# Performance work log

Measured on AMD Instinct MI355X. Metric: run time of the kernel, lower is better.

## Reference

```python
import jax, jax.numpy as jnp
import numpy as np


def _cdist(p1, p2):
    # Euclidean cdist via the matmul expansion (matches torch.cdist p=2 fast path):
    # ||a-b||^2 = ||a||^2 + ||b||^2 - 2 a.b ; clamp tiny negatives before sqrt.
    sq1 = jnp.sum(p1 * p1, axis=-1, keepdims=True)        # (N, 1)
    sq2 = jnp.sum(p2 * p2, axis=-1, keepdims=True).T      # (1, M)
    d2 = sq1 + sq2 - 2.0 * (p1 @ p2.T)                    # (N, M)
    return jnp.sqrt(jnp.maximum(d2, 0.0))


def setup_inputs() -> dict:
    key = jax.random.key(0)
    k1, k2 = jax.random.split(key)
    N, M = 16384, 16384
    points1 = jax.random.normal(k1, (N, 3), dtype=jnp.float32)
    points2 = jax.random.normal(k2, (M, 3), dtype=jnp.float32)
    return {"points1": points1, "points2": points2}


def reference(points1, points2):
    dist = _cdist(points1, points2)                        # (N, M)
    min1 = jnp.min(dist, axis=1)                           # (N,) nearest in points2
    min2 = jnp.min(dist, axis=0)                           # (M,) nearest in points1
    return jnp.sum(min1) + jnp.sum(min2)
```

## Files before the change

kernel.cpp:

```cpp
#include <hip/hip_runtime.h>
#include <math.h>


typedef _Float16 half8    __attribute__((ext_vector_type(8)));
typedef float    floatx16 __attribute__((ext_vector_type(16)));

constexpr int NPTS = 16384;
constexpr int ROWS = 128;
constexpr int BLK  = 1024;

__device__ __forceinline__ uint2 pack_point(const float* __restrict__ P, int j)
{
    float x = P[3*j], y = P[3*j+1], z = P[3*j+2];
    _Float16 hx = (_Float16)x, hy = (_Float16)y, hz = (_Float16)z;
    float qx = (float)hx, qy = (float)hy, qz = (float)hz;
    _Float16 hw = (_Float16)(qx*qx + qy*qy + qz*qz);
    union { _Float16 h[4]; uint2 u; } p;
    p.h[0] = hx; p.h[1] = hy; p.h[2] = hz; p.h[3] = hw;
    return p.u;
}

__global__ __launch_bounds__(BLK, 4) void chamfer_all_kernel(
    const float* __restrict__ P1, const float* __restrict__ P2,
    float* __restrict__ out, int n1, int n2)
{
    __shared__ uint2 sB[NPTS];
    __shared__ float sRowMin[4][ROWS];
    __shared__ float sRed[ROWS];

    const int dir   = blockIdx.z;
    const float* PA = dir == 0 ? P1 : P2;
    const float* PB = dir == 0 ? P2 : P1;
    const int nA    = dir == 0 ? n1 : n2;
    const int nB    = dir == 0 ? n2 : n1;

    const int tid  = threadIdx.x;
    const int wave = tid >> 6;
    const int lane = tid & 63;
    const int n    = lane & 31;
    const int g    = lane >> 5;
    const bool g0  = (g == 0);
    const int wr   = wave & 3;
    const int wq   = wave >> 2;

    for (int j = tid; j < NPTS; j += BLK) {
        int jj = j < nB ? j : nB - 1;
        sB[j] = pack_point(PB, jj);
    }

    const _Float16 h0 = (_Float16)0.0f;
    half8 af;
    {
        int arow = blockIdx.x * ROWS + wr * 32 + n;
        int j = arow < nA ? arow : nA - 1;
        union { uint2 u; _Float16 h[4]; } au; au.u = pack_point(PA, j);
        const _Float16 m2 = (_Float16)(-2.0f);
        af[0] = g0 ? (_Float16)(au.h[0] * m2) : h0;
        af[1] = g0 ? (_Float16)(au.h[1] * m2) : h0;
        af[2] = g0 ? (_Float16)(au.h[2] * m2) : h0;
        af[3] = g0 ? (_Float16)1.0f : h0;
        af[4] = g0 ? au.h[3] : h0;
        af[5] = h0; af[6] = h0; af[7] = h0;
    }

    __syncthreads();

    floatx16 rowmin;
#pragma unroll
    for (int r = 0; r < 16; ++r) rowmin[r] = 1e30f;
    const floatx16 zacc = {};

    union BF { half8 v; unsigned u[4]; uint2 lo; };
    BF bu0, bu1;
    { union { _Float16 h[2]; unsigned u; } q;
      q.h[0] = (_Float16)1.0f; q.h[1] = h0;
      bu0.u[2] = q.u; bu0.u[3] = 0u;
      bu1.u[2] = q.u; bu1.u[3] = 0u; }

    constexpr int QLEN = NPTS >> 2;
    constexpr int NT   = QLEN / 64;
    const uint2* qbase = sB + wq * QLEN + n;
    uint2 c0 = qbase[0], c1 = qbase[32];

    for (int bt = 0; bt < NT; ++bt) {
        const uint2* pn = qbase + (bt + 1 < NT ? (bt + 1) * 64 : 0);
        uint2 f0 = pn[0], f1 = pn[32];

        bu0.lo = c0;
        bu1.lo = c1;

        floatx16 d0 = __builtin_amdgcn_mfma_f32_32x32x16_f16(af, bu0.v, zacc, 0, 0, 0);
        floatx16 d1 = __builtin_amdgcn_mfma_f32_32x32x16_f16(af, bu1.v, zacc, 0, 0, 0);

#pragma unroll
        for (int r = 0; r < 16; ++r)
            rowmin[r] = fminf(fminf(rowmin[r], d0[r]), d1[r]);

        c0 = f0; c1 = f1;
    }

#pragma unroll
    for (int mask = 1; mask <= 16; mask <<= 1)
#pragma unroll
        for (int r = 0; r < 16; ++r)
            rowmin[r] = fminf(rowmin[r], __shfl_xor(rowmin[r], mask));

    if (n == 0) {
#pragma unroll
        for (int r = 0; r < 16; ++r) {
            int rr = wr * 32 + g * 4 + ((r & 3) + 8 * (r >> 2));
            sRowMin[wq][rr] = rowmin[r];
        }
    }
    __syncthreads();

    if (tid < ROWS) {
        float m = fminf(fminf(sRowMin[0][tid], sRowMin[1][tid]),
                        fminf(sRowMin[2][tid], sRowMin[3][tid]));
        int grow = blockIdx.x * ROWS + tid;
        sRed[tid] = (grow < nA) ? sqrtf(fmaxf(m, 0.0f)) : 0.0f;
    }
    __syncthreads();

    if (tid < 64) {
        float v = sRed[tid] + sRed[tid + 64];
#pragma unroll
        for (int mask = 1; mask <= 32; mask <<= 1)
            v += __shfl_xor(v, mask);
        if (tid == 0) atomicAdd(out, v);
    }
}

extern "C" void kernel_launch(void* const* d_in, const int* in_sizes, int n_in,
                              void* d_out, int out_size, void* d_ws, size_t ws_size,
                              hipStream_t stream) {
    const float* P1 = (const float*)d_in[0];
    const float* P2 = (const float*)d_in[1];
    const int n1 = in_sizes[0] / 3;
    const int n2 = in_sizes[1] / 3;
    float* out = (float*)d_out;

    hipMemsetAsync(out, 0, sizeof(float), stream);

    dim3 grid(NPTS / ROWS, 1, 2);
    chamfer_all_kernel<<<grid, BLK, 0, stream>>>(P1, P2, out, n1, n2);
}
```

Before: 78.13 us.

## Split B-point sweep into halves with partial mins and separate reduce kernel

Each block now loads only half of the opposing point set (8192 points) into shared memory, and the grid doubles along y to cover both halves. Per-row partial minima go to a workspace buffer, and a second kernel combines the two halves, applies sqrt and does the sum with atomics. This halves LDS use per block, doubles block count, and raises the launch-bounds occupancy hint, so more blocks can be resident. The cost is an extra kernel launch, a workspace round-trip, and removal of the software prefetch in the inner loop.

```diff
diff --git a/kernel.cpp b/kernel.cpp
--- a/kernel.cpp
+++ b/kernel.cpp
@@ -6,6 +6,7 @@
 typedef float    floatx16 __attribute__((ext_vector_type(16)));
 
 constexpr int NPTS = 16384;
+constexpr int HALF = 8192;
 constexpr int ROWS = 128;
 constexpr int BLK  = 1024;
 
@@ -20,15 +21,15 @@
     return p.u;
 }
 
-__global__ __launch_bounds__(BLK, 4) void chamfer_all_kernel(
+__global__ __launch_bounds__(BLK, 8) void chamfer_sweep_kernel(
     const float* __restrict__ P1, const float* __restrict__ P2,
-    float* __restrict__ out, int n1, int n2)
+    float* __restrict__ part, int n1, int n2)
 {
-    __shared__ uint2 sB[NPTS];
+    __shared__ uint2 sB[HALF];
     __shared__ float sRowMin[4][ROWS];
-    __shared__ float sRed[ROWS];
 
     const int dir   = blockIdx.z;
+    const int half  = blockIdx.y;
     const float* PA = dir == 0 ? P1 : P2;
     const float* PB = dir == 0 ? P2 : P1;
     const int nA    = dir == 0 ? n1 : n2;
@@ -43,8 +44,9 @@
     const int wr   = wave & 3;
     const int wq   = wave >> 2;
 
-    for (int j = tid; j < NPTS; j += BLK) {
-        int jj = j < nB ? j : nB - 1;
+    for (int j = tid; j < HALF; j += BLK) {
+        int jg = half * HALF + j;
+        int jj = jg < nB ? jg : nB - 1;
         sB[j] = pack_point(PB, jj);
     }
 
@@ -77,26 +79,21 @@
       bu0.u[2] = q.u; bu0.u[3] = 0u;
       bu1.u[2] = q.u; bu1.u[3] = 0u; }
 
-    constexpr int QLEN = NPTS >> 2;
+    constexpr int QLEN = HALF >> 2;
     constexpr int NT   = QLEN / 64;
     const uint2* qbase = sB + wq * QLEN + n;
-    uint2 c0 = qbase[0], c1 = qbase[32];
+    for (int bt = 0; bt < NT; ++bt) {
+        const uint2* p = qbase + bt * 64;
+        bu0.lo = p[0];
+        bu1.lo = p[32];
 
-    for (int bt = 0; bt < NT; ++bt) {
-        const uint2* pn = qbase + (bt + 1 < NT ? (bt + 1) * 64 : 0);
-        uint2 f0 = pn[0], f1 = pn[32];
+        floatx16 d = __builtin_amdgcn_mfma_f32_32x32x16_f16(af, bu0.v, zacc, 0, 0, 0);
+#pragma unroll
+        for (int r = 0; r < 16; ++r) rowmin[r] = fminf(rowmin[r], d[r]);
 
-        bu0.lo = c0;
-        bu1.lo = c1;
-
-        floatx16 d0 = __builtin_amdgcn_mfma_f32_32x32x16_f16(af, bu0.v, zacc, 0, 0, 0);
-        floatx16 d1 = __builtin_amdgcn_mfma_f32_32x32x16_f16(af, bu1.v, zacc, 0, 0, 0);
-
+        d = __builtin_amdgcn_mfma_f32_32x32x16_f16(af, bu1.v, zacc, 0, 0, 0);
 #pragma unroll
-        for (int r = 0; r < 16; ++r)
-            rowmin[r] = fminf(fminf(rowmin[r], d0[r]), d1[r]);
-
-        c0 = f0; c1 = f1;
+        for (int r = 0; r < 16; ++r) rowmin[r] = fminf(rowmin[r], d[r]);
     }
 
 #pragma unroll
@@ -118,17 +115,30 @@
         float m = fminf(fminf(sRowMin[0][tid], sRowMin[1][tid]),
                         fminf(sRowMin[2][tid], sRowMin[3][tid]));
         int grow = blockIdx.x * ROWS + tid;
-        sRed[tid] = (grow < nA) ? sqrtf(fmaxf(m, 0.0f)) : 0.0f;
+        if (grow < nA)
+            part[(size_t)(((dir << 14) + grow) << 1) + half] = m;
     }
+}
+
+__global__ __launch_bounds__(256) void reduce_kernel(
+    const float* __restrict__ part, float* __restrict__ out,
+    int n1, int n2)
+{
+    __shared__ float s[256];
+    int rr = blockIdx.x * 256 + threadIdx.x;
+    int dir = rr >> 14, row = rr & 16383;
+    float acc = 0.0f;
+    if (row < (dir == 0 ? n1 : n2)) {
+        const float2 v = ((const float2*)part)[rr];
+        acc = sqrtf(fmaxf(fminf(v.x, v.y), 0.0f));
+    }
+    s[threadIdx.x] = acc;
     __syncthreads();
-
-    if (tid < 64) {
-        float v = sRed[tid] + sRed[tid + 64];
-#pragma unroll
-        for (int mask = 1; mask <= 32; mask <<= 1)
-            v += __shfl_xor(v, mask);
-        if (tid == 0) atomicAdd(out, v);
+    for (int w = 128; w > 0; w >>= 1) {
+        if (threadIdx.x < w) s[threadIdx.x] += s[threadIdx.x + w];
+        __syncthreads();
     }
+    if (threadIdx.x == 0) atomicAdd(out, s[0]);
 }
 
 extern "C" void kernel_launch(void* const* d_in, const int* in_sizes, int n_in,
@@ -138,10 +148,14 @@
     const float* P2 = (const float*)d_in[1];
     const int n1 = in_sizes[0] / 3;
     const int n2 = in_sizes[1] / 3;
-    float* out = (float*)d_out;
+    float* part = (float*)d_ws;
+    float* out  = (float*)d_out;
 
     hipMemsetAsync(out, 0, sizeof(float), stream);
 
-    dim3 grid(NPTS / ROWS, 1, 2);
-    chamfer_all_kernel<<<grid, BLK, 0, stream>>>(P1, P2, out, n1, n2);
+    {
+        dim3 grid(NPTS / ROWS, 2, 2);
+        chamfer_sweep_kernel<<<grid, BLK, 0, stream>>>(P1, P2, part, n1, n2);
+    }
+    reduce_kernel<<<(2 * NPTS) / 256, 256, 0, stream>>>(part, out, n1, n2);
 }
```

Result: slower. 81.24 us (+4.0%).

## Software-pipeline MFMA and min-fold with inline asm and sched barriers

Applied to the files above, without the earlier changes.

Restructures the inner loop into a two-stage ping-pong so the MFMAs for tile t+1 are issued before the min-fold of tile t's results. Inline asm MFMAs and sched_barrier stop the compiler from serialising the fold behind the MFMA latency. The aim is to hide MFMA latency behind VALU fminf work. The cost is more accumulator registers live at once, which could reduce occupancy. Inline asm also skips the compiler's hazard handling, so correctness depends on the hardware resolving MFMA result dependencies.

```diff
diff --git a/kernel.cpp b/kernel.cpp
--- a/kernel.cpp
+++ b/kernel.cpp
@@ -68,7 +68,9 @@
     floatx16 rowmin;
 #pragma unroll
     for (int r = 0; r < 16; ++r) rowmin[r] = 1e30f;
-    const floatx16 zacc = {};
+    floatx16 zacc;
+#pragma unroll
+    for (int r = 0; r < 16; ++r) zacc[r] = 0.0f;
 
     union BF { half8 v; unsigned u[4]; uint2 lo; };
     BF bu0, bu1;
@@ -79,25 +81,40 @@
 
     constexpr int QLEN = NPTS >> 2;
     constexpr int NT   = QLEN / 64;
-    const uint2* qbase = sB + wq * QLEN + n;
-    uint2 c0 = qbase[0], c1 = qbase[32];
+    const uint2* qb = sB + wq * QLEN + n;
 
-    for (int bt = 0; bt < NT; ++bt) {
-        const uint2* pn = qbase + (bt + 1 < NT ? (bt + 1) * 64 : 0);
-        uint2 f0 = pn[0], f1 = pn[32];
+#define LOADB(t)  do { bu0.lo = qb[(t) * 64]; bu1.lo = qb[(t) * 64 + 32]; } while (0)
+#define MFMA_PAIR(D0, D1) do { \
+    asm("v_mfma_f32_32x32x16_f16 %0, %1, %2, %3" \
+        : "=&v"(D0) : "v"(af), "v"(bu0.v), "v"(zacc)); \
+    asm("v_mfma_f32_32x32x16_f16 %0, %1, %2, %3" \
+        : "=&v"(D1) : "v"(af), "v"(bu1.v), "v"(zacc)); } while (0)
+#define FOLD(P0, P1) do { \
+    _Pragma("unroll") \
+    for (int r = 0; r < 16; ++r) \
+        rowmin[r] = fminf(fminf(rowmin[r], (P0)[r]), (P1)[r]); } while (0)
 
-        bu0.lo = c0;
-        bu1.lo = c1;
-
-        floatx16 d0 = __builtin_amdgcn_mfma_f32_32x32x16_f16(af, bu0.v, zacc, 0, 0, 0);
-        floatx16 d1 = __builtin_amdgcn_mfma_f32_32x32x16_f16(af, bu1.v, zacc, 0, 0, 0);
-
-#pragma unroll
-        for (int r = 0; r < 16; ++r)
-            rowmin[r] = fminf(fminf(rowmin[r], d0[r]), d1[r]);
-
-        c0 = f0; c1 = f1;
+    floatx16 pA0, pA1, pB0, pB1;
+    LOADB(0);
+    MFMA_PAIR(pA0, pA1);
+    for (int t = 1; t < NT - 1; t += 2) {
+        LOADB(t);
+        MFMA_PAIR(pB0, pB1);
+        __builtin_amdgcn_sched_barrier(0);
+        FOLD(pA0, pA1);
+        LOADB(t + 1);
+        MFMA_PAIR(pA0, pA1);
+        __builtin_amdgcn_sched_barrier(0);
+        FOLD(pB0, pB1);
     }
+    LOADB(NT - 1);
+    MFMA_PAIR(pB0, pB1);
+    __builtin_amdgcn_sched_barrier(0);
+    FOLD(pA0, pA1);
+    FOLD(pB0, pB1);
+#undef LOADB
+#undef MFMA_PAIR
+#undef FOLD
 
 #pragma unroll
     for (int mask = 1; mask <= 16; mask <<= 1)
```

New measurement: 77.06 us. Within noise of the previous version (-1.4%).

## Hand-schedule MFMA/min inner loop in inline asm with double-buffered B fragments

Applied to the files above, without the earlier changes.

Replaces the compiler-generated inner loop with inline assembly that pins MFMA outputs and B fragments to fixed VGPRs. LDS reads for the next tile are issued before the min3 fold of the previous MFMA results, and the loop alternates between two B register sets. The constant 1.0/0 halves of the B fragments are written once instead of every iteration. The code hardcodes register numbers and uses s_nop padding for MFMA result hazards, so correctness depends on the exact register clobbers and hazard timing.

```diff
diff --git a/kernel.cpp b/kernel.cpp
--- a/kernel.cpp
+++ b/kernel.cpp
@@ -19,6 +19,91 @@
     p.h[0] = hx; p.h[1] = hy; p.h[2] = hz; p.h[3] = hw;
     return p.u;
 }
+
+#define CLB "v32","v33","v34","v35","v36","v37","v38","v39", \
+            "v40","v41","v42","v43","v44","v45","v46","v47", \
+            "v48","v49","v50","v51","v52","v53","v54","v55", \
+            "v56","v57","v58","v59","v60","v61","v62","v63", \
+            "v64","v65","v66","v67","v68","v69","v70","v71", \
+            "v72","v73","v74","v75","v76","v77","v78","v79"
+
+#define PRO_ASM \
+    "ds_read_b64 v[64:65], %0\n\t" \
+    "ds_read_b64 v[68:69], %0 offset:256\n\t" \
+    "v_mov_b32 v66, 0x3c00\n\t" \
+    "v_mov_b32 v67, 0\n\t" \
+    "v_mov_b32 v70, 0x3c00\n\t" \
+    "v_mov_b32 v71, 0\n\t" \
+    "v_mov_b32 v74, 0x3c00\n\t" \
+    "v_mov_b32 v75, 0\n\t" \
+    "v_mov_b32 v78, 0x3c00\n\t" \
+    "v_mov_b32 v79, 0\n\t" \
+    "v_add_u32 %0, 512, %0\n\t" \
+    "s_waitcnt lgkmcnt(0)\n\t" \
+    "v_mfma_f32_32x32x16_f16 v[32:47], %1, v[64:67], %2\n\t" \
+    "v_mfma_f32_32x32x16_f16 v[48:63], %1, v[68:71], %2"
+
+#define FOLD16 \
+    "v_min3_f32 %1, %1, v32, v48\n\t" \
+    "v_min3_f32 %2, %2, v33, v49\n\t" \
+    "v_min3_f32 %3, %3, v34, v50\n\t" \
+    "v_min3_f32 %4, %4, v35, v51\n\t" \
+    "v_min3_f32 %5, %5, v36, v52\n\t" \
+    "v_min3_f32 %6, %6, v37, v53\n\t" \
+    "v_min3_f32 %7, %7, v38, v54\n\t" \
+    "v_min3_f32 %8, %8, v39, v55\n\t" \
+    "v_min3_f32 %9, %9, v40, v56\n\t" \
+    "v_min3_f32 %10, %10, v41, v57\n\t" \
+    "v_min3_f32 %11, %11, v42, v58\n\t" \
+    "v_min3_f32 %12, %12, v43, v59\n\t" \
+    "v_min3_f32 %13, %13, v44, v60\n\t" \
+    "v_min3_f32 %14, %14, v45, v61\n\t" \
+    "v_min3_f32 %15, %15, v46, v62\n\t" \
+    "v_min3_f32 %16, %16, v47, v63\n\t"
+
+#define STEP_O_ASM \
+    "ds_read_b64 v[72:73], %0\n\t" \
+    "ds_read_b64 v[76:77], %0 offset:256\n\t" \
+    "v_add_u32 %0, 512, %0\n\t" \
+    "s_nop 7\n\t" "s_nop 7\n\t" "s_nop 7\n\t" "s_nop 7\n\t" \
+    FOLD16 \
+    "s_waitcnt lgkmcnt(0)\n\t" \
+    "v_mfma_f32_32x32x16_f16 v[32:47], %17, v[72:75], %18\n\t" \
+    "v_mfma_f32_32x32x16_f16 v[48:63], %17, v[76:79], %18"
+
+#define STEP_E_ASM \
+    "ds_read_b64 v[64:65], %0\n\t" \
+    "ds_read_b64 v[68:69], %0 offset:256\n\t" \
+    "v_add_u32 %0, 512, %0\n\t" \
+    "s_nop 7\n\t" "s_nop 7\n\t" "s_nop 7\n\t" "s_nop 7\n\t" \
+    FOLD16 \
+    "s_waitcnt lgkmcnt(0)\n\t" \
+    "v_mfma_f32_32x32x16_f16 v[32:47], %17, v[64:67], %18\n\t" \
+    "v_mfma_f32_32x32x16_f16 v[48:63], %17, v[68:71], %18"
+
+#define FIN_ASM \
+    "s_nop 7\n\t" "s_nop 7\n\t" "s_nop 7\n\t" "s_nop 7\n\t" \
+    "v_min3_f32 %0, %0, v32, v48\n\t" \
+    "v_min3_f32 %1, %1, v33, v49\n\t" \
+    "v_min3_f32 %2, %2, v34, v50\n\t" \
+    "v_min3_f32 %3, %3, v35, v51\n\t" \
+    "v_min3_f32 %4, %4, v36, v52\n\t" \
+    "v_min3_f32 %5, %5, v37, v53\n\t" \
+    "v_min3_f32 %6, %6, v38, v54\n\t" \
+    "v_min3_f32 %7, %7, v39, v55\n\t" \
+    "v_min3_f32 %8, %8, v40, v56\n\t" \
+    "v_min3_f32 %9, %9, v41, v57\n\t" \
+    "v_min3_f32 %10, %10, v42, v58\n\t" \
+    "v_min3_f32 %11, %11, v43, v59\n\t" \
+    "v_min3_f32 %12, %12, v44, v60\n\t" \
+    "v_min3_f32 %13, %13, v45, v61\n\t" \
+    "v_min3_f32 %14, %14, v46, v62\n\t" \
+    "v_min3_f32 %15, %15, v47, v63"
+
+#define RM_OUTS "+v"(rm0), "+v"(rm1), "+v"(rm2), "+v"(rm3), \
+                "+v"(rm4), "+v"(rm5), "+v"(rm6), "+v"(rm7), \
+                "+v"(rm8), "+v"(rm9), "+v"(rm10), "+v"(rm11), \
+                "+v"(rm12), "+v"(rm13), "+v"(rm14), "+v"(rm15)
 
 __global__ __launch_bounds__(BLK, 4) void chamfer_all_kernel(
     const float* __restrict__ P1, const float* __restrict__ P2,
@@ -65,39 +150,31 @@
 
     __syncthreads();
 
-    floatx16 rowmin;
-#pragma unroll
-    for (int r = 0; r < 16; ++r) rowmin[r] = 1e30f;
-    const floatx16 zacc = {};
-
-    union BF { half8 v; unsigned u[4]; uint2 lo; };
-    BF bu0, bu1;
-    { union { _Float16 h[2]; unsigned u; } q;
-      q.h[0] = (_Float16)1.0f; q.h[1] = h0;
-      bu0.u[2] = q.u; bu0.u[3] = 0u;
-      bu1.u[2] = q.u; bu1.u[3] = 0u; }
+    floatx16 zacc;
+#pragma unroll
+    for (int r = 0; r < 16; ++r) zacc[r] = 0.0f;
+
+    float rm0 = 1e30f, rm1 = 1e30f, rm2 = 1e30f, rm3 = 1e30f,
+          rm4 = 1e30f, rm5 = 1e30f, rm6 = 1e30f, rm7 = 1e30f,
+          rm8 = 1e30f, rm9 = 1e30f, rm10 = 1e30f, rm11 = 1e30f,
+          rm12 = 1e30f, rm13 = 1e30f, rm14 = 1e30f, rm15 = 1e30f;
 
     constexpr int QLEN = NPTS >> 2;
-    constexpr int NT   = QLEN / 64;
-    const uint2* qbase = sB + wq * QLEN + n;
-    uint2 c0 = qbase[0], c1 = qbase[32];
-
-    for (int bt = 0; bt < NT; ++bt) {
-        const uint2* pn = qbase + (bt + 1 < NT ? (bt + 1) * 64 : 0);
-        uint2 f0 = pn[0], f1 = pn[32];
-
-        bu0.lo = c0;
-        bu1.lo = c1;
-
-        floatx16 d0 = __builtin_amdgcn_mfma_f32_32x32x16_f16(af, bu0.v, zacc, 0, 0, 0);
-        floatx16 d1 = __builtin_amdgcn_mfma_f32_32x32x16_f16(af, bu1.v, zacc, 0, 0, 0);
-
-#pragma unroll
-        for (int r = 0; r < 16; ++r)
-            rowmin[r] = fminf(fminf(rowmin[r], d0[r]), d1[r]);
-
-        c0 = f0; c1 = f1;
-    }
+    unsigned aaddr = (unsigned)(size_t)(sB + wq * QLEN + n);
+
+    asm volatile(PRO_ASM : "+v"(aaddr) : "v"(af), "v"(zacc) : CLB, "memory");
+    for (int it = 0; it < 31; ++it) {
+        asm volatile(STEP_O_ASM
+            : "+v"(aaddr), RM_OUTS : "v"(af), "v"(zacc) : CLB, "memory");
+        asm volatile(STEP_E_ASM
+            : "+v"(aaddr), RM_OUTS : "v"(af), "v"(zacc) : CLB, "memory");
+    }
+    asm volatile(STEP_O_ASM
+        : "+v"(aaddr), RM_OUTS : "v"(af), "v"(zacc) : CLB, "memory");
+    asm volatile(FIN_ASM : RM_OUTS : : CLB);
+
+    float rowmin[16] = { rm0, rm1, rm2, rm3, rm4, rm5, rm6, rm7,
+                         rm8, rm9, rm10, rm11, rm12, rm13, rm14, rm15 };
 
 #pragma unroll
     for (int mask = 1; mask <= 16; mask <<= 1)
```

New measurement: 79.80 us. 2.1% more time.
